# Kernel optimization log

Measured on AMD Instinct MI355X. Metric: run time of the kernel, lower is better.

## Reference

```python
import jax, jax.numpy as jnp
import numpy as np

PROJ_EPS = 1e-5   # hyperbolic_projection keeps ||x|| <= 1 - PROJ_EPS
MIN_NORM = 1e-15  # numerical floor for norms/denominators
N, D, E, L = 100000, 128, 800000, 2


def _norm(x):
    return jnp.linalg.norm(x, axis=-1, keepdims=True)


def hyperbolic_projection(x):
    n = _norm(x)
    max_n = 1.0 - PROJ_EPS
    scale = jnp.where(n > max_n, max_n / jnp.maximum(n, MIN_NORM), 1.0)
    return x * scale


def exp_map_zero(v):
    n = jnp.maximum(_norm(v), MIN_NORM)
    return jnp.tanh(n) * v / n


def log_map_zero(y):
    n = jnp.maximum(_norm(y), MIN_NORM)
    nc = jnp.clip(n, MIN_NORM, 1.0 - PROJ_EPS)
    return jnp.arctanh(nc) * y / n


def mobius_addition(u, v):
    uu = jnp.sum(u * u, -1, keepdims=True)
    vv = jnp.sum(v * v, -1, keepdims=True)
    uv = jnp.sum(u * v, -1, keepdims=True)
    num = (1.0 + 2.0 * uv + vv) * u + (1.0 - uu) * v
    den = 1.0 + 2.0 * uv + uu * vv
    return num / jnp.maximum(den, MIN_NORM)


def setup_inputs() -> dict:
    key = jax.random.key(0)
    k = jax.random.split(key, 5)
    ent = jax.random.normal(k[0], (N, D), jnp.float32) * 0.1
    W = jax.random.normal(k[1], (L, D, D), jnp.float32) * (1.0 / np.sqrt(D))
    bias = jnp.zeros((L, D), jnp.float32)
    rows = jax.random.randint(k[2], (E,), 0, N)
    cols = jax.random.randint(k[3], (E,), 0, N)
    vals = jax.random.uniform(k[4], (E,), jnp.float32) / 8.0  # ~row-normalized adj values
    return {"ent_embeddings": ent, "W": W, "bias": bias,
            "adj_rows": rows, "adj_cols": cols, "adj_vals": vals}


def _gcn_layer(x, W_l, b_l, rows, cols, vals, use_act):
    # log map to tangent at origin, linear transform
    t = log_map_zero(x)                      # [N, D]
    m = t @ W_l                              # [N, D]
    # sparse adjacency matmul: adj @ m  (COO gather-scale-scatter)
    msg = m[cols] * vals[:, None]            # [E, D]
    agg = jax.ops.segment_sum(msg, rows, num_segments=N)  # [N, D]
    h = hyperbolic_projection(exp_map_zero(agg))
    # hyperbolic bias via mobius addition
    bh = hyperbolic_projection(exp_map_zero(b_l[None, :]))  # [1, D]
    h = hyperbolic_projection(mobius_addition(h, bh))
    if use_act:
        h = hyperbolic_projection(exp_map_zero(jnp.tanh(log_map_zero(h))))
    return h


def reference(ent_embeddings, W, bias, adj_rows, adj_cols, adj_vals):
    x = hyperbolic_projection(ent_embeddings)
    for l in range(L):
        use_act = (l < L - 1)  # tanh on all but last layer
        h = _gcn_layer(x, W[l], bias[l], adj_rows, adj_cols, adj_vals, use_act)
        # mobius residual connection with previous layer output
        x = hyperbolic_projection(mobius_addition(h, x))
    return x
```

## Files before the change

kernel.cpp:

```cpp
#include <hip/hip_runtime.h>
#include <math.h>

#define D 128
#define PROJ_EPS 1e-5f
#define MAX_NN (1.0f - PROJ_EPS)
#define MIN_NORM 1e-15f
#define ROWS_PER_BLOCK 2048
#define BSHIFT 11
#define MAXB 256

struct __align__(8) Edge { int c; float v; };

typedef __attribute__((ext_vector_type(8))) short bf16x8;
typedef __attribute__((ext_vector_type(4))) float f32x4;

__device__ inline unsigned cvt_pk_bf16(float a, float b) {
    unsigned r;
    asm("v_cvt_pk_bf16_f32 %0, %1, %2" : "=v"(r) : "v"(a), "v"(b));
    return r;
}

__device__ inline float wave_sum(float v) {
#pragma unroll
    for (int off = 32; off; off >>= 1) v += __shfl_xor(v, off, 64);
    return v;
}
__device__ inline float g16sum(float v) {
#pragma unroll
    for (int off = 8; off; off >>= 1) v += __shfl_xor(v, off, 64);
    return v;
}
__device__ inline void g16sum2(float& a, float& b) {
#pragma unroll
    for (int off = 8; off; off >>= 1) {
        a += __shfl_xor(a, off, 64);
        b += __shfl_xor(b, off, 64);
    }
}
__device__ inline float frcp(float x) { return __builtin_amdgcn_rcpf(x); }
__device__ inline float fsqrt_(float x) { return __builtin_amdgcn_sqrtf(x); }
__device__ inline float tanh_pos(float x) {
    float e = __expf(-2.f * x);
    return (1.f - e) * frcp(1.f + e);
}
__device__ inline float tanh_sgn(float x) {
    float ax = fabsf(x);
    float e = __expf(-2.f * ax);
    float r = (1.f - e) * frcp(1.f + e);
    return copysignf(r, x);
}
__device__ inline float atanh_clip(float x) {
    return 0.5f * __logf((1.f + x) * frcp(1.f - x));
}

__device__ inline float2 mk2(float a, float b) { float2 r; r.x = a; r.y = b; return r; }
__device__ inline float2 bc2(float a) { return mk2(a, a); }
__device__ inline float2 pk_fma2(float2 a, float2 b, float2 c) {
    float2 d;
    asm("v_pk_fma_f32 %0, %1, %2, %3" : "=v"(d) : "v"(a), "v"(b), "v"(c));
    return d;
}
__device__ inline float2 pk_mul2(float2 a, float2 b) {
    float2 d;
    asm("v_pk_mul_f32 %0, %1, %2" : "=v"(d) : "v"(a), "v"(b));
    return d;
}
__device__ inline float2 up2(unsigned u) {
    uint2 t; t.x = u << 16; t.y = u & 0xffff0000u;
    float2 r; r.x = __uint_as_float(t.x); r.y = __uint_as_float(t.y);
    return r;
}

__global__ __launch_bounds__(256) void hist_kernel(const int* __restrict__ rows,
                                                   int* __restrict__ counts,
                                                   int* __restrict__ bucket_cnt, int e) {
    __shared__ int bhist[MAXB];
    int t = threadIdx.x;
    if (t < MAXB) bhist[t] = 0;
    __syncthreads();
    int base = blockIdx.x * 2048;
#pragma unroll
    for (int j = 0; j < 8; ++j) {
        int i = base + t * 8 + j;
        if (i < e) {
            int r = rows[i];
            atomicAdd(&counts[r], 1);
            atomicAdd(&bhist[r >> BSHIFT], 1);
        }
    }
    __syncthreads();
    if (t < MAXB && bhist[t]) atomicAdd(&bucket_cnt[t], bhist[t]);
}

__global__ __launch_bounds__(256) void partial_kernel(const int* __restrict__ counts,
                                                      int* __restrict__ partials, int n) {
    int t = threadIdx.x;
    int start = blockIdx.x * ROWS_PER_BLOCK + t * 8;
    int s = 0;
#pragma unroll
    for (int j = 0; j < 8; ++j) {
        int i = start + j;
        if (i < n) s += (counts[i] + 3) & ~3;
    }
    int lane = t & 63, wv = t >> 6;
#pragma unroll
    for (int o = 32; o; o >>= 1) s += __shfl_xor(s, o, 64);
    __shared__ int wsum[4];
    if (lane == 0) wsum[wv] = s;
    __syncthreads();
    if (t == 0) partials[blockIdx.x] = wsum[0] + wsum[1] + wsum[2] + wsum[3];
}

__global__ void scan_both(int* __restrict__ partials, int npart,
                          const int* __restrict__ bucket_cnt, int* __restrict__ bucket_cur) {
    __shared__ int buf[1024];
    int t = threadIdx.x;
    int v = (t < npart) ? partials[t] : 0;
    buf[t] = v;
    __syncthreads();
    for (int o = 1; o < 1024; o <<= 1) {
        int x = (t >= o) ? buf[t - o] : 0;
        __syncthreads();
        buf[t] += x;
        __syncthreads();
    }
    if (t < npart) partials[t] = buf[t] - v;
    __syncthreads();
    int b = (t < npart) ? bucket_cnt[t] : 0;
    buf[t] = b;
    __syncthreads();
    for (int o = 1; o < 1024; o <<= 1) {
        int x = (t >= o) ? buf[t - o] : 0;
        __syncthreads();
        buf[t] += x;
        __syncthreads();
    }
    if (t < npart) bucket_cur[t] = buf[t] - b;
}

__global__ __launch_bounds__(256) void rowptr_kernel(const int* __restrict__ counts,
                                                     const int* __restrict__ partials,
                                                     int* __restrict__ row_ptr,
                                                     int* __restrict__ cursor, int n) {
    int t = threadIdx.x;
    int start = blockIdx.x * ROWS_PER_BLOCK + t * 8;
    int c[8];
    int s = 0;
#pragma unroll
    for (int j = 0; j < 8; ++j) {
        int i = start + j;
        c[j] = (i < n) ? ((counts[i] + 3) & ~3) : 0;
        s += c[j];
    }
    int lane = t & 63, wv = t >> 6;
    int inc = s;
#pragma unroll
    for (int o = 1; o < 64; o <<= 1) {
        int tt = __shfl_up(inc, o, 64);
        if (lane >= o) inc += tt;
    }
    __shared__ int wsum[4];
    if (lane == 63) wsum[wv] = inc;
    __syncthreads();
    if (t == 0) {
        int acc = 0;
        for (int w = 0; w < 4; ++w) { int tmp = wsum[w]; wsum[w] = acc; acc += tmp; }
    }
    __syncthreads();
    int run = partials[blockIdx.x] + wsum[wv] + (inc - s);
#pragma unroll
    for (int j = 0; j < 8; ++j) {
        int i = start + j;
        if (i < n) {
            row_ptr[i] = run;
            cursor[i] = run;
            run += c[j];
            if (i == n - 1) row_ptr[n] = run;
        }
    }
}

__global__ __launch_bounds__(256) void bucket_scatter(const int* __restrict__ rows,
                                                      const int* __restrict__ cols,
                                                      const float* __restrict__ vals,
                                                      int* __restrict__ bucket_cur,
                                                      int* __restrict__ rstage,
                                                      Edge* __restrict__ estage, int e) {
    __shared__ int bhist[MAXB];
    __shared__ int bbase[MAXB];
    int t = threadIdx.x;
    if (t < MAXB) bhist[t] = 0;
    __syncthreads();
    int base = blockIdx.x * 2048;
    int b[8], lr[8];
#pragma unroll
    for (int j = 0; j < 8; ++j) {
        int i = base + t * 8 + j;
        if (i < e) {
            b[j] = rows[i] >> BSHIFT;
            lr[j] = atomicAdd(&bhist[b[j]], 1);
        } else b[j] = -1;
    }
    __syncthreads();
    if (t < MAXB) {
        int c = bhist[t];
        bbase[t] = c ? atomicAdd(&bucket_cur[t], c) : 0;
    }
    __syncthreads();
#pragma unroll
    for (int j = 0; j < 8; ++j) {
        int i = base + t * 8 + j;
        if (b[j] >= 0) {
            int pos = bbase[b[j]] + lr[j];
            rstage[pos] = rows[i];
            Edge ed; ed.c = cols[i]; ed.v = vals[i];
            estage[pos] = ed;
        }
    }
}

__global__ void scatter2(const int* __restrict__ rstage, const Edge* __restrict__ estage,
                         int* __restrict__ cursor, Edge* __restrict__ eds, int e) {
    int i = blockIdx.x * blockDim.x + threadIdx.x;
    if (i < e) {
        int r = rstage[i];
        int pos = atomicAdd(&cursor[r], 1);
        eds[pos] = estage[i];
    }
}

__global__ __launch_bounds__(256) void proj_init(const float* __restrict__ ent,
                                                 float* __restrict__ x,
                                                 float* __restrict__ logscale,
                                                 float* __restrict__ xnorm2, int n) {
    int wv = (int)((blockIdx.x * (size_t)blockDim.x + threadIdx.x) >> 6);
    int lane = threadIdx.x & 63;
    int q = lane >> 4, li = lane & 15;
    if (wv * 4 >= n) return;
    int r = wv * 4 + q;
    bool active = (r < n);
    float4 va = active ? *(const float4*)(ent + (size_t)r * D + 8 * li)
                       : make_float4(0.f, 0.f, 0.f, 0.f);
    float4 vb = active ? *(const float4*)(ent + (size_t)r * D + 8 * li + 4)
                       : make_float4(0.f, 0.f, 0.f, 0.f);
    float ss = va.x * va.x + va.y * va.y + va.z * va.z + va.w * va.w
             + vb.x * vb.x + vb.y * vb.y + vb.z * vb.z + vb.w * vb.w;
    ss = g16sum(ss);
    float nrm = fsqrt_(ss);
    float scale = (nrm > MAX_NN) ? MAX_NN * frcp(fmaxf(nrm, MIN_NORM)) : 1.0f;
    float n2 = fminf(nrm, MAX_NN);
    float nc = fminf(fmaxf(n2, MIN_NORM), MAX_NN);
    float ls = atanh_clip(nc) * frcp(fmaxf(n2, MIN_NORM));
    if (active) {
        *(float4*)(x + (size_t)r * D + 8 * li) =
            make_float4(va.x * scale, va.y * scale, va.z * scale, va.w * scale);
        *(float4*)(x + (size_t)r * D + 8 * li + 4) =
            make_float4(vb.x * scale, vb.y * scale, vb.z * scale, vb.w * scale);
        if (li == 0) { logscale[r] = ls; xnorm2[r] = n2 * n2; }
    }
}

__global__ void bias_prep(const float* __restrict__ bias, float* __restrict__ bh,
                          float* __restrict__ vvb) {
    int l = blockIdx.x;
    int lane = threadIdx.x;
    float2 b2 = *(const float2*)(bias + (size_t)l * D + 2 * lane);
    float nn = fmaxf(sqrtf(wave_sum(b2.x * b2.x + b2.y * b2.y)), MIN_NORM);
    float s = tanhf(nn) / nn;
    float bx = b2.x * s, by = b2.y * s;
    float pn = sqrtf(wave_sum(bx * bx + by * by));
    float sc = (pn > MAX_NN) ? MAX_NN / fmaxf(pn, MIN_NORM) : 1.0f;
    bx *= sc; by *= sc;
    float vv = wave_sum(bx * bx + by * by);
    *(float2*)(bh + (size_t)l * D + 2 * lane) = make_float2(bx, by);
    if (lane == 0) vvb[l] = vv;
}

__global__ __launch_bounds__(256, 3) void logmap_gemm(const float* __restrict__ x,
                                                      const float* __restrict__ logscale,
                                                      const float* __restrict__ W,
                                                      unsigned short* __restrict__ m, int n,
                                                      int ntiles) {
    __shared__ char lds[16384];
    const int t = threadIdx.x;
    const int wid = t >> 6, lane = t & 63;
    const int lcol = lane & 15, lkg = lane >> 4;
    const int colbase = wid * 32;

    bf16x8 Bh[4][2], Bl[4][2];
#pragma unroll
    for (int ki = 0; ki < 4; ++ki) {
#pragma unroll
        for (int cf = 0; cf < 2; ++cf) {
            const float* wp = W + (size_t)(ki * 32 + lkg * 8) * D + colbase + cf * 16 + lcol;
            float f[8];
#pragma unroll
            for (int e2 = 0; e2 < 8; ++e2) f[e2] = wp[(size_t)e2 * D];
            unsigned hw[4], lw[4];
#pragma unroll
            for (int p = 0; p < 4; ++p) {
                float a = f[2 * p], b = f[2 * p + 1];
                unsigned h = cvt_pk_bf16(a, b);
                float ha = __uint_as_float(h << 16);
                float hb = __uint_as_float(h & 0xffff0000u);
                hw[p] = h;
                lw[p] = cvt_pk_bf16(a - ha, b - hb);
            }
            uint4 uh = make_uint4(hw[0], hw[1], hw[2], hw[3]);
            uint4 ul = make_uint4(lw[0], lw[1], lw[2], lw[3]);
            Bh[ki][cf] = *(bf16x8*)&uh;
            Bl[ki][cf] = *(bf16x8*)&ul;
        }
    }

    for (int tile = blockIdx.x; tile < ntiles; tile += gridDim.x) {
        const int row0 = tile * 32;
        __syncthreads();
#pragma unroll
        for (int p = t; p < 512; p += 256) {
            int fi = p >> 6, ln = p & 63;
            int rf = fi >> 2, ki = fi & 3;
            int row = row0 + rf * 16 + (ln & 15);
            int k0 = ki * 32 + (ln >> 4) * 8;
            float v[8];
            if (row < n) {
                float ls = logscale[row];
                const float* xp = x + (size_t)row * D + k0;
                *(float4*)&v[0] = *(const float4*)xp;
                *(float4*)&v[4] = *(const float4*)(xp + 4);
#pragma unroll
                for (int e2 = 0; e2 < 8; ++e2) v[e2] *= ls;
            } else {
#pragma unroll
                for (int e2 = 0; e2 < 8; ++e2) v[e2] = 0.f;
            }
            unsigned hv[4], lv[4];
#pragma unroll
            for (int pp = 0; pp < 4; ++pp) {
                float a = v[2 * pp], b = v[2 * pp + 1];
                unsigned h = cvt_pk_bf16(a, b);
                float ha = __uint_as_float(h << 16);
                float hb = __uint_as_float(h & 0xffff0000u);
                hv[pp] = h;
                lv[pp] = cvt_pk_bf16(a - ha, b - hb);
            }
            *(uint4*)(lds + fi * 1024 + ln * 16) = make_uint4(hv[0], hv[1], hv[2], hv[3]);
            *(uint4*)(lds + 8192 + fi * 1024 + ln * 16) = make_uint4(lv[0], lv[1], lv[2], lv[3]);
        }
        __syncthreads();

        f32x4 acc[2][2];
#pragma unroll
        for (int cf = 0; cf < 2; ++cf)
#pragma unroll
            for (int rf = 0; rf < 2; ++rf) acc[cf][rf] = (f32x4){0.f, 0.f, 0.f, 0.f};

#pragma unroll
        for (int ki = 0; ki < 4; ++ki) {
            bf16x8 Ah[2], Al[2];
#pragma unroll
            for (int rf = 0; rf < 2; ++rf) {
                Ah[rf] = *(const bf16x8*)(lds + (rf * 4 + ki) * 1024 + lane * 16);
                Al[rf] = *(const bf16x8*)(lds + 8192 + (rf * 4 + ki) * 1024 + lane * 16);
            }
#pragma unroll
            for (int cf = 0; cf < 2; ++cf)
#pragma unroll
                for (int rf = 0; rf < 2; ++rf) {
                    acc[cf][rf] = __builtin_amdgcn_mfma_f32_16x16x32_bf16(Bh[ki][cf], Ah[rf], acc[cf][rf], 0, 0, 0);
                    acc[cf][rf] = __builtin_amdgcn_mfma_f32_16x16x32_bf16(Bl[ki][cf], Ah[rf], acc[cf][rf], 0, 0, 0);
                    acc[cf][rf] = __builtin_amdgcn_mfma_f32_16x16x32_bf16(Bh[ki][cf], Al[rf], acc[cf][rf], 0, 0, 0);
                }
        }

#pragma unroll
        for (int cf = 0; cf < 2; ++cf)
#pragma unroll
            for (int rf = 0; rf < 2; ++rf) {
                int mrow = row0 + rf * 16 + lcol;
                if (mrow < n) {
                    unsigned u0 = cvt_pk_bf16(acc[cf][rf][0], acc[cf][rf][1]);
                    unsigned u1 = cvt_pk_bf16(acc[cf][rf][2], acc[cf][rf][3]);
                    *(uint2*)(m + (size_t)mrow * D + colbase + cf * 16 + lkg * 4) =
                        make_uint2(u0, u1);
                }
            }
    }
}

__global__ __launch_bounds__(256) void aggregate(const unsigned short* __restrict__ m,
                                                 const int* __restrict__ row_ptr,
                                                 const Edge* __restrict__ eds,
                                                 const float* __restrict__ bh,
                                                 const float* __restrict__ vvb_p,
                                                 float* __restrict__ x,
                                                 float* __restrict__ logscale,
                                                 float* __restrict__ xnorm2,
                                                 int n, int use_act, int last) {
    int wv = (int)((blockIdx.x * (size_t)blockDim.x + threadIdx.x) >> 6);
    int lane = threadIdx.x & 63;
    int q = lane >> 4, li = lane & 15;
    if (wv * 4 >= n) return;
    int r = wv * 4 + q;
    bool active = (r < n);

    int beg = 0, end = 0;
    if (active) { beg = row_ptr[r]; end = row_ptr[r + 1]; }

    float vv = active ? xnorm2[r] : 0.f;
    float4 xa = active ? *(const float4*)(x + (size_t)r * D + 8 * li)
                       : make_float4(0.f, 0.f, 0.f, 0.f);
    float4 xb = active ? *(const float4*)(x + (size_t)r * D + 8 * li + 4)
                       : make_float4(0.f, 0.f, 0.f, 0.f);

    const char* mB = (const char*)m + ((size_t)li << 4);
    float2 A01 = bc2(0.f), A23 = bc2(0.f), A45 = bc2(0.f), A67 = bc2(0.f);
    int e = beg;
    for (; e + 8 <= end; e += 8) {
#pragma unroll
        for (int j = 0; j < 8; ++j) {
            Edge ee = eds[e + j];
            uint4 g = *(const uint4*)(mB + ((size_t)(unsigned)ee.c << 8));
            float2 v = bc2(ee.v);
            A01 = pk_fma2(up2(g.x), v, A01); A23 = pk_fma2(up2(g.y), v, A23);
            A45 = pk_fma2(up2(g.z), v, A45); A67 = pk_fma2(up2(g.w), v, A67);
        }
    }
    if (e < end) {
#pragma unroll
        for (int j = 0; j < 4; ++j) {
            Edge ee = eds[e + j];
            uint4 g = *(const uint4*)(mB + ((size_t)(unsigned)ee.c << 8));
            float2 v = bc2(ee.v);
            A01 = pk_fma2(up2(g.x), v, A01); A23 = pk_fma2(up2(g.y), v, A23);
            A45 = pk_fma2(up2(g.z), v, A45); A67 = pk_fma2(up2(g.w), v, A67);
        }
    }

    float4 bv0 = *(const float4*)(bh + 8 * li);
    float4 bv1 = *(const float4*)(bh + 8 * li + 4);
    float2 b01 = mk2(bv0.x, bv0.y), b23 = mk2(bv0.z, bv0.w);
    float2 b45 = mk2(bv1.x, bv1.y), b67 = mk2(bv1.z, bv1.w);
    float vvb = *vvb_p;

    float2 daa = pk_fma2(A67, A67, pk_fma2(A45, A45, pk_fma2(A23, A23, pk_mul2(A01, A01))));
    float2 dab = pk_fma2(A67, b67, pk_fma2(A45, b45, pk_fma2(A23, b23, pk_mul2(A01, b01))));
    float saa = daa.x + daa.y, sab = dab.x + dab.y;
    g16sum2(saa, sab);

    float na = fmaxf(fsqrt_(saa), MIN_NORM);
    float th = tanh_pos(na);
    float s1 = th * frcp(na);
    float nh = th;
    if (th > MAX_NN) { s1 *= MAX_NN * frcp(th); nh = MAX_NN; }
    float2 vs1 = bc2(s1);
    float2 H01 = pk_mul2(A01, vs1), H23 = pk_mul2(A23, vs1);
    float2 H45 = pk_mul2(A45, vs1), H67 = pk_mul2(A67, vs1);
    float uu = nh * nh;
    float uv = s1 * sab;

    float ca = 1.f + 2.f * uv + vvb;
    float cb = 1.f - uu;
    float den = fmaxf(1.f + 2.f * uv + uu * vvb, MIN_NORM);
    float nsq = fmaxf(ca * ca * uu + 2.f * ca * cb * uv + cb * cb * vvb, 0.f);
    float rden = frcp(den);
    float n2 = fsqrt_(nsq) * rden;
    float s2 = rden;
    if (n2 > MAX_NN) { s2 *= MAX_NN * frcp(n2); n2 = MAX_NN; }
    float2 vca = bc2(ca), vcb = bc2(cb), vs2 = bc2(s2);
    float2 P01 = pk_mul2(pk_fma2(H01, vca, pk_mul2(b01, vcb)), vs2);
    float2 P23 = pk_mul2(pk_fma2(H23, vca, pk_mul2(b23, vcb)), vs2);
    float2 P45 = pk_mul2(pk_fma2(H45, vca, pk_mul2(b45, vcb)), vs2);
    float2 P67 = pk_mul2(pk_fma2(H67, vca, pk_mul2(b67, vcb)), vs2);

    float2 xo01 = mk2(xa.x, xa.y), xo23 = mk2(xa.z, xa.w);
    float2 xo45 = mk2(xb.x, xb.y), xo67 = mk2(xb.z, xb.w);

    float2 Q01, Q23, Q45, Q67;
    float uu3, uv3;
    if (use_act) {
        float nnv = fmaxf(n2, MIN_NORM);
        float nc = fminf(fmaxf(n2, MIN_NORM), MAX_NN);
        float ls2 = atanh_clip(nc) * frcp(nnv);
        float2 vls = bc2(ls2);
        float2 Z01 = pk_mul2(P01, vls), Z23 = pk_mul2(P23, vls);
        float2 Z45 = pk_mul2(P45, vls), Z67 = pk_mul2(P67, vls);
        float2 T01 = mk2(tanh_sgn(Z01.x), tanh_sgn(Z01.y));
        float2 T23 = mk2(tanh_sgn(Z23.x), tanh_sgn(Z23.y));
        float2 T45 = mk2(tanh_sgn(Z45.x), tanh_sgn(Z45.y));
        float2 T67 = mk2(tanh_sgn(Z67.x), tanh_sgn(Z67.y));
        float2 dtt = pk_fma2(T67, T67, pk_fma2(T45, T45, pk_fma2(T23, T23, pk_mul2(T01, T01))));
        float2 dtx = pk_fma2(T67, xo67, pk_fma2(T45, xo45, pk_fma2(T23, xo23, pk_mul2(T01, xo01))));
        float stt = dtt.x + dtt.y, stx = dtx.x + dtx.y;
        g16sum2(stt, stx);
        float n3 = fmaxf(fsqrt_(stt), MIN_NORM);
        float th3 = tanh_pos(n3);
        float s3 = th3 * frcp(n3);
        float nh3 = th3;
        if (th3 > MAX_NN) { s3 *= MAX_NN * frcp(th3); nh3 = MAX_NN; }
        float2 vs3 = bc2(s3);
        Q01 = pk_mul2(T01, vs3); Q23 = pk_mul2(T23, vs3);
        Q45 = pk_mul2(T45, vs3); Q67 = pk_mul2(T67, vs3);
        uu3 = nh3 * nh3;
        uv3 = s3 * stx;
    } else {
        float2 dpx = pk_fma2(P67, xo67, pk_fma2(P45, xo45, pk_fma2(P23, xo23, pk_mul2(P01, xo01))));
        float suv = g16sum(dpx.x + dpx.y);
        Q01 = P01; Q23 = P23; Q45 = P45; Q67 = P67;
        uu3 = n2 * n2;
        uv3 = suv;
    }

    ca = 1.f + 2.f * uv3 + vv;
    cb = 1.f - uu3;
    den = fmaxf(1.f + 2.f * uv3 + uu3 * vv, MIN_NORM);
    nsq = fmaxf(ca * ca * uu3 + 2.f * ca * cb * uv3 + cb * cb * vv, 0.f);
    rden = frcp(den);
    float n4 = fsqrt_(nsq) * rden;
    float s4 = rden;
    if (n4 > MAX_NN) { s4 *= MAX_NN * frcp(n4); n4 = MAX_NN; }
    float2 vca2 = bc2(ca), vcb2 = bc2(cb), vs4 = bc2(s4);
    float2 O01 = pk_mul2(pk_fma2(Q01, vca2, pk_mul2(xo01, vcb2)), vs4);
    float2 O23 = pk_mul2(pk_fma2(Q23, vca2, pk_mul2(xo23, vcb2)), vs4);
    float2 O45 = pk_mul2(pk_fma2(Q45, vca2, pk_mul2(xo45, vcb2)), vs4);
    float2 O67 = pk_mul2(pk_fma2(Q67, vca2, pk_mul2(xo67, vcb2)), vs4);

    if (active) {
        *(float4*)(x + (size_t)r * D + 8 * li) = make_float4(O01.x, O01.y, O23.x, O23.y);
        *(float4*)(x + (size_t)r * D + 8 * li + 4) = make_float4(O45.x, O45.y, O67.x, O67.y);
        if (li == 0) {
            xnorm2[r] = n4 * n4;
            if (!last) {
                float nnv = fmaxf(n4, MIN_NORM);
                float nc = fminf(fmaxf(n4, MIN_NORM), MAX_NN);
                logscale[r] = atanh_clip(nc) * frcp(nnv);
            }
        }
    }
}

extern "C" void kernel_launch(void* const* d_in, const int* in_sizes, int n_in,
                              void* d_out, int out_size, void* d_ws, size_t ws_size,
                              hipStream_t stream) {
    const float* ent  = (const float*)d_in[0];
    const float* W    = (const float*)d_in[1];
    const float* bias = (const float*)d_in[2];
    const int* rows   = (const int*)d_in[3];
    const int* cols   = (const int*)d_in[4];
    const float* vals = (const float*)d_in[5];
    float* x = (float*)d_out;

    const int n = in_sizes[0] / D;
    const int e = in_sizes[3];
    const int nlayers = in_sizes[1] / (D * D);
    const int npart = (n + ROWS_PER_BLOCK - 1) / ROWS_PER_BLOCK;
    const int npart_e = (e + 2047) / 2048;
    const int ntiles = (n + 31) / 32;
    const size_t e_cap = (size_t)e + 3u * (size_t)n;

    char* ws = (char*)d_ws;
    size_t off = 0;
    auto alloc = [&](size_t bytes) {
        void* p = ws + off;
        off += (bytes + 255) & ~(size_t)255;
        return p;
    };
    unsigned short* m = (unsigned short*)alloc((size_t)n * D * sizeof(unsigned short));
    float* logscale = (float*)alloc((size_t)n * sizeof(float));
    float* xnorm2   = (float*)alloc((size_t)n * sizeof(float));
    int*   counts   = (int*)alloc((size_t)n * sizeof(int));
    int*   row_ptr  = (int*)alloc((size_t)(n + 1) * sizeof(int));
    int*   cursor   = (int*)alloc((size_t)n * sizeof(int));
    int*   partials = (int*)alloc((size_t)(npart > 1024 ? npart : 1024) * sizeof(int));
    int*   bucket_cnt = (int*)alloc((size_t)MAXB * sizeof(int));
    int*   bucket_cur = (int*)alloc((size_t)MAXB * sizeof(int));
    float* bhb      = (float*)alloc((size_t)nlayers * D * sizeof(float));
    float* vvb      = (float*)alloc((size_t)nlayers * sizeof(float));
    int*   rstage   = (int*)alloc((size_t)e * sizeof(int));
    Edge*  estage   = (Edge*)alloc((size_t)e * sizeof(Edge));
    Edge*  eds      = (Edge*)alloc(e_cap * sizeof(Edge));

    hipMemsetAsync(counts, 0, (size_t)n * sizeof(int), stream);
    hipMemsetAsync(bucket_cnt, 0, (size_t)MAXB * sizeof(int), stream);
    hipMemsetAsync(eds, 0, e_cap * sizeof(Edge), stream);

    hist_kernel<<<npart_e, 256, 0, stream>>>(rows, counts, bucket_cnt, e);
    partial_kernel<<<npart, 256, 0, stream>>>(counts, partials, n);
    scan_both<<<1, 1024, 0, stream>>>(partials, npart, bucket_cnt, bucket_cur);
    rowptr_kernel<<<npart, 256, 0, stream>>>(counts, partials, row_ptr, cursor, n);
    bucket_scatter<<<npart_e, 256, 0, stream>>>(rows, cols, vals, bucket_cur, rstage, estage, e);
    scatter2<<<(e + 255) / 256, 256, 0, stream>>>(rstage, estage, cursor, eds, e);

    bias_prep<<<nlayers, 64, 0, stream>>>(bias, bhb, vvb);
    proj_init<<<(n + 15) / 16, 256, 0, stream>>>(ent, x, logscale, xnorm2, n);

    for (int l = 0; l < nlayers; ++l) {
        logmap_gemm<<<782, 256, 0, stream>>>(x, logscale, W + (size_t)l * D * D, m, n, ntiles);
        int use_act = (l < nlayers - 1) ? 1 : 0;
        aggregate<<<(n + 15) / 16, 256, 0, stream>>>(m, row_ptr, eds, bhb + (size_t)l * D,
                                                     vvb + l, x, logscale, xnorm2, n,
                                                     use_act, (l == nlayers - 1) ? 1 : 0);
    }
}
```

Baseline: 275.4 us.

## Fuse GEMM into aggregation by reordering adj@(tW) to (adj@t)W

Uses associativity to aggregate the bf16 tangent vectors first and then multiply the aggregated 16-row tile by W with MFMA inside the aggregation kernel. This removes the separate logmap_gemm launch and the round trip of the m buffer. The previous layer writes the log-mapped tangent directly in bf16, double-buffered. In exchange, the per-tile GEMM adds three syncthreads per 16 rows. Inputs to the aggregation are now bf16-rounded tangents rather than bf16 GEMM outputs, which shifts where rounding error enters.

```diff
diff --git a/kernel.cpp b/kernel.cpp
--- a/kernel.cpp
+++ b/kernel.cpp
@@ -231,7 +231,7 @@
 
 __global__ __launch_bounds__(256) void proj_init(const float* __restrict__ ent,
                                                  float* __restrict__ x,
-                                                 float* __restrict__ logscale,
+                                                 unsigned short* __restrict__ t_out,
                                                  float* __restrict__ xnorm2, int n) {
     int wv = (int)((blockIdx.x * (size_t)blockDim.x + threadIdx.x) >> 6);
     int lane = threadIdx.x & 63;
@@ -252,11 +252,16 @@
     float nc = fminf(fmaxf(n2, MIN_NORM), MAX_NN);
     float ls = atanh_clip(nc) * frcp(fmaxf(n2, MIN_NORM));
     if (active) {
-        *(float4*)(x + (size_t)r * D + 8 * li) =
-            make_float4(va.x * scale, va.y * scale, va.z * scale, va.w * scale);
-        *(float4*)(x + (size_t)r * D + 8 * li + 4) =
-            make_float4(vb.x * scale, vb.y * scale, vb.z * scale, vb.w * scale);
-        if (li == 0) { logscale[r] = ls; xnorm2[r] = n2 * n2; }
+        float p0 = va.x * scale, p1 = va.y * scale, p2 = va.z * scale, p3 = va.w * scale;
+        float p4 = vb.x * scale, p5 = vb.y * scale, p6 = vb.z * scale, p7 = vb.w * scale;
+        *(float4*)(x + (size_t)r * D + 8 * li) = make_float4(p0, p1, p2, p3);
+        *(float4*)(x + (size_t)r * D + 8 * li + 4) = make_float4(p4, p5, p6, p7);
+        unsigned w0 = cvt_pk_bf16(p0 * ls, p1 * ls);
+        unsigned w1 = cvt_pk_bf16(p2 * ls, p3 * ls);
+        unsigned w2 = cvt_pk_bf16(p4 * ls, p5 * ls);
+        unsigned w3 = cvt_pk_bf16(p6 * ls, p7 * ls);
+        *(uint4*)(t_out + (size_t)r * D + 8 * li) = make_uint4(w0, w1, w2, w3);
+        if (li == 0) xnorm2[r] = n2 * n2;
     }
 }
 
@@ -276,18 +281,26 @@
     if (lane == 0) vvb[l] = vv;
 }
 
-__global__ __launch_bounds__(256, 3) void logmap_gemm(const float* __restrict__ x,
-                                                      const float* __restrict__ logscale,
-                                                      const float* __restrict__ W,
-                                                      unsigned short* __restrict__ m, int n,
-                                                      int ntiles) {
-    __shared__ char lds[16384];
+__global__ __launch_bounds__(256) void fused_layer(const unsigned short* __restrict__ t_in,
+                                                   float* __restrict__ x,
+                                                   float* __restrict__ xnorm2,
+                                                   const int* __restrict__ row_ptr,
+                                                   const Edge* __restrict__ eds,
+                                                   const float* __restrict__ bh,
+                                                   const float* __restrict__ vvb_p,
+                                                   const float* __restrict__ W,
+                                                   unsigned short* __restrict__ t_out,
+                                                   int n, int ntile, int use_act, int last) {
+    __shared__ char ufrag[8192];
+    __shared__ float gbuf[16][136];
+
     const int t = threadIdx.x;
-    const int wid = t >> 6, lane = t & 63;
+    const int w = t >> 6, lane = t & 63;
     const int lcol = lane & 15, lkg = lane >> 4;
-    const int colbase = wid * 32;
-
-    bf16x8 Bh[4][2], Bl[4][2];
+    const int q = lkg & 3, li = lcol;
+    const int colbase = w * 32;
+
+    bf16x8 Wh[4][2], Wl[4][2];
 #pragma unroll
     for (int ki = 0; ki < 4; ++ki) {
 #pragma unroll
@@ -308,132 +321,8 @@
             }
             uint4 uh = make_uint4(hw[0], hw[1], hw[2], hw[3]);
             uint4 ul = make_uint4(lw[0], lw[1], lw[2], lw[3]);
-            Bh[ki][cf] = *(bf16x8*)&uh;
-            Bl[ki][cf] = *(bf16x8*)&ul;
-        }
-    }
-
-    for (int tile = blockIdx.x; tile < ntiles; tile += gridDim.x) {
-        const int row0 = tile * 32;
-        __syncthreads();
-#pragma unroll
-        for (int p = t; p < 512; p += 256) {
-            int fi = p >> 6, ln = p & 63;
-            int rf = fi >> 2, ki = fi & 3;
-            int row = row0 + rf * 16 + (ln & 15);
-            int k0 = ki * 32 + (ln >> 4) * 8;
-            float v[8];
-            if (row < n) {
-                float ls = logscale[row];
-                const float* xp = x + (size_t)row * D + k0;
-                *(float4*)&v[0] = *(const float4*)xp;
-                *(float4*)&v[4] = *(const float4*)(xp + 4);
-#pragma unroll
-                for (int e2 = 0; e2 < 8; ++e2) v[e2] *= ls;
-            } else {
-#pragma unroll
-                for (int e2 = 0; e2 < 8; ++e2) v[e2] = 0.f;
-            }
-            unsigned hv[4], lv[4];
-#pragma unroll
-            for (int pp = 0; pp < 4; ++pp) {
-                float a = v[2 * pp], b = v[2 * pp + 1];
-                unsigned h = cvt_pk_bf16(a, b);
-                float ha = __uint_as_float(h << 16);
-                float hb = __uint_as_float(h & 0xffff0000u);
-                hv[pp] = h;
-                lv[pp] = cvt_pk_bf16(a - ha, b - hb);
-            }
-            *(uint4*)(lds + fi * 1024 + ln * 16) = make_uint4(hv[0], hv[1], hv[2], hv[3]);
-            *(uint4*)(lds + 8192 + fi * 1024 + ln * 16) = make_uint4(lv[0], lv[1], lv[2], lv[3]);
-        }
-        __syncthreads();
-
-        f32x4 acc[2][2];
-#pragma unroll
-        for (int cf = 0; cf < 2; ++cf)
-#pragma unroll
-            for (int rf = 0; rf < 2; ++rf) acc[cf][rf] = (f32x4){0.f, 0.f, 0.f, 0.f};
-
-#pragma unroll
-        for (int ki = 0; ki < 4; ++ki) {
-            bf16x8 Ah[2], Al[2];
-#pragma unroll
-            for (int rf = 0; rf < 2; ++rf) {
-                Ah[rf] = *(const bf16x8*)(lds + (rf * 4 + ki) * 1024 + lane * 16);
-                Al[rf] = *(const bf16x8*)(lds + 8192 + (rf * 4 + ki) * 1024 + lane * 16);
-            }
-#pragma unroll
-            for (int cf = 0; cf < 2; ++cf)
-#pragma unroll
-                for (int rf = 0; rf < 2; ++rf) {
-                    acc[cf][rf] = __builtin_amdgcn_mfma_f32_16x16x32_bf16(Bh[ki][cf], Ah[rf], acc[cf][rf], 0, 0, 0);
-                    acc[cf][rf] = __builtin_amdgcn_mfma_f32_16x16x32_bf16(Bl[ki][cf], Ah[rf], acc[cf][rf], 0, 0, 0);
-                    acc[cf][rf] = __builtin_amdgcn_mfma_f32_16x16x32_bf16(Bh[ki][cf], Al[rf], acc[cf][rf], 0, 0, 0);
-                }
-        }
-
-#pragma unroll
-        for (int cf = 0; cf < 2; ++cf)
-#pragma unroll
-            for (int rf = 0; rf < 2; ++rf) {
-                int mrow = row0 + rf * 16 + lcol;
-                if (mrow < n) {
-                    unsigned u0 = cvt_pk_bf16(acc[cf][rf][0], acc[cf][rf][1]);
-                    unsigned u1 = cvt_pk_bf16(acc[cf][rf][2], acc[cf][rf][3]);
-                    *(uint2*)(m + (size_t)mrow * D + colbase + cf * 16 + lkg * 4) =
-                        make_uint2(u0, u1);
-                }
-            }
-    }
-}
-
-__global__ __launch_bounds__(256) void aggregate(const unsigned short* __restrict__ m,
-                                                 const int* __restrict__ row_ptr,
-                                                 const Edge* __restrict__ eds,
-                                                 const float* __restrict__ bh,
-                                                 const float* __restrict__ vvb_p,
-                                                 float* __restrict__ x,
-                                                 float* __restrict__ logscale,
-                                                 float* __restrict__ xnorm2,
-                                                 int n, int use_act, int last) {
-    int wv = (int)((blockIdx.x * (size_t)blockDim.x + threadIdx.x) >> 6);
-    int lane = threadIdx.x & 63;
-    int q = lane >> 4, li = lane & 15;
-    if (wv * 4 >= n) return;
-    int r = wv * 4 + q;
-    bool active = (r < n);
-
-    int beg = 0, end = 0;
-    if (active) { beg = row_ptr[r]; end = row_ptr[r + 1]; }
-
-    float vv = active ? xnorm2[r] : 0.f;
-    float4 xa = active ? *(const float4*)(x + (size_t)r * D + 8 * li)
-                       : make_float4(0.f, 0.f, 0.f, 0.f);
-    float4 xb = active ? *(const float4*)(x + (size_t)r * D + 8 * li + 4)
-                       : make_float4(0.f, 0.f, 0.f, 0.f);
-
-    const char* mB = (const char*)m + ((size_t)li << 4);
-    float2 A01 = bc2(0.f), A23 = bc2(0.f), A45 = bc2(0.f), A67 = bc2(0.f);
-    int e = beg;
-    for (; e + 8 <= end; e += 8) {
-#pragma unroll
-        for (int j = 0; j < 8; ++j) {
-            Edge ee = eds[e + j];
-            uint4 g = *(const uint4*)(mB + ((size_t)(unsigned)ee.c << 8));
-            float2 v = bc2(ee.v);
-            A01 = pk_fma2(up2(g.x), v, A01); A23 = pk_fma2(up2(g.y), v, A23);
-            A45 = pk_fma2(up2(g.z), v, A45); A67 = pk_fma2(up2(g.w), v, A67);
-        }
-    }
-    if (e < end) {
-#pragma unroll
-        for (int j = 0; j < 4; ++j) {
-            Edge ee = eds[e + j];
-            uint4 g = *(const uint4*)(mB + ((size_t)(unsigned)ee.c << 8));
-            float2 v = bc2(ee.v);
-            A01 = pk_fma2(up2(g.x), v, A01); A23 = pk_fma2(up2(g.y), v, A23);
-            A45 = pk_fma2(up2(g.z), v, A45); A67 = pk_fma2(up2(g.w), v, A67);
+            Wh[ki][cf] = *(bf16x8*)&uh;
+            Wl[ki][cf] = *(bf16x8*)&ul;
         }
     }
 
@@ -443,99 +332,184 @@
     float2 b45 = mk2(bv1.x, bv1.y), b67 = mk2(bv1.z, bv1.w);
     float vvb = *vvb_p;
 
-    float2 daa = pk_fma2(A67, A67, pk_fma2(A45, A45, pk_fma2(A23, A23, pk_mul2(A01, A01))));
-    float2 dab = pk_fma2(A67, b67, pk_fma2(A45, b45, pk_fma2(A23, b23, pk_mul2(A01, b01))));
-    float saa = daa.x + daa.y, sab = dab.x + dab.y;
-    g16sum2(saa, sab);
-
-    float na = fmaxf(fsqrt_(saa), MIN_NORM);
-    float th = tanh_pos(na);
-    float s1 = th * frcp(na);
-    float nh = th;
-    if (th > MAX_NN) { s1 *= MAX_NN * frcp(th); nh = MAX_NN; }
-    float2 vs1 = bc2(s1);
-    float2 H01 = pk_mul2(A01, vs1), H23 = pk_mul2(A23, vs1);
-    float2 H45 = pk_mul2(A45, vs1), H67 = pk_mul2(A67, vs1);
-    float uu = nh * nh;
-    float uv = s1 * sab;
-
-    float ca = 1.f + 2.f * uv + vvb;
-    float cb = 1.f - uu;
-    float den = fmaxf(1.f + 2.f * uv + uu * vvb, MIN_NORM);
-    float nsq = fmaxf(ca * ca * uu + 2.f * ca * cb * uv + cb * cb * vvb, 0.f);
-    float rden = frcp(den);
-    float n2 = fsqrt_(nsq) * rden;
-    float s2 = rden;
-    if (n2 > MAX_NN) { s2 *= MAX_NN * frcp(n2); n2 = MAX_NN; }
-    float2 vca = bc2(ca), vcb = bc2(cb), vs2 = bc2(s2);
-    float2 P01 = pk_mul2(pk_fma2(H01, vca, pk_mul2(b01, vcb)), vs2);
-    float2 P23 = pk_mul2(pk_fma2(H23, vca, pk_mul2(b23, vcb)), vs2);
-    float2 P45 = pk_mul2(pk_fma2(H45, vca, pk_mul2(b45, vcb)), vs2);
-    float2 P67 = pk_mul2(pk_fma2(H67, vca, pk_mul2(b67, vcb)), vs2);
-
-    float2 xo01 = mk2(xa.x, xa.y), xo23 = mk2(xa.z, xa.w);
-    float2 xo45 = mk2(xb.x, xb.y), xo67 = mk2(xb.z, xb.w);
-
-    float2 Q01, Q23, Q45, Q67;
-    float uu3, uv3;
-    if (use_act) {
-        float nnv = fmaxf(n2, MIN_NORM);
-        float nc = fminf(fmaxf(n2, MIN_NORM), MAX_NN);
-        float ls2 = atanh_clip(nc) * frcp(nnv);
-        float2 vls = bc2(ls2);
-        float2 Z01 = pk_mul2(P01, vls), Z23 = pk_mul2(P23, vls);
-        float2 Z45 = pk_mul2(P45, vls), Z67 = pk_mul2(P67, vls);
-        float2 T01 = mk2(tanh_sgn(Z01.x), tanh_sgn(Z01.y));
-        float2 T23 = mk2(tanh_sgn(Z23.x), tanh_sgn(Z23.y));
-        float2 T45 = mk2(tanh_sgn(Z45.x), tanh_sgn(Z45.y));
-        float2 T67 = mk2(tanh_sgn(Z67.x), tanh_sgn(Z67.y));
-        float2 dtt = pk_fma2(T67, T67, pk_fma2(T45, T45, pk_fma2(T23, T23, pk_mul2(T01, T01))));
-        float2 dtx = pk_fma2(T67, xo67, pk_fma2(T45, xo45, pk_fma2(T23, xo23, pk_mul2(T01, xo01))));
-        float stt = dtt.x + dtt.y, stx = dtx.x + dtx.y;
-        g16sum2(stt, stx);
-        float n3 = fmaxf(fsqrt_(stt), MIN_NORM);
-        float th3 = tanh_pos(n3);
-        float s3 = th3 * frcp(n3);
-        float nh3 = th3;
-        if (th3 > MAX_NN) { s3 *= MAX_NN * frcp(th3); nh3 = MAX_NN; }
-        float2 vs3 = bc2(s3);
-        Q01 = pk_mul2(T01, vs3); Q23 = pk_mul2(T23, vs3);
-        Q45 = pk_mul2(T45, vs3); Q67 = pk_mul2(T67, vs3);
-        uu3 = nh3 * nh3;
-        uv3 = s3 * stx;
-    } else {
-        float2 dpx = pk_fma2(P67, xo67, pk_fma2(P45, xo45, pk_fma2(P23, xo23, pk_mul2(P01, xo01))));
-        float suv = g16sum(dpx.x + dpx.y);
-        Q01 = P01; Q23 = P23; Q45 = P45; Q67 = P67;
-        uu3 = n2 * n2;
-        uv3 = suv;
-    }
-
-    ca = 1.f + 2.f * uv3 + vv;
-    cb = 1.f - uu3;
-    den = fmaxf(1.f + 2.f * uv3 + uu3 * vv, MIN_NORM);
-    nsq = fmaxf(ca * ca * uu3 + 2.f * ca * cb * uv3 + cb * cb * vv, 0.f);
-    rden = frcp(den);
-    float n4 = fsqrt_(nsq) * rden;
-    float s4 = rden;
-    if (n4 > MAX_NN) { s4 *= MAX_NN * frcp(n4); n4 = MAX_NN; }
-    float2 vca2 = bc2(ca), vcb2 = bc2(cb), vs4 = bc2(s4);
-    float2 O01 = pk_mul2(pk_fma2(Q01, vca2, pk_mul2(xo01, vcb2)), vs4);
-    float2 O23 = pk_mul2(pk_fma2(Q23, vca2, pk_mul2(xo23, vcb2)), vs4);
-    float2 O45 = pk_mul2(pk_fma2(Q45, vca2, pk_mul2(xo45, vcb2)), vs4);
-    float2 O67 = pk_mul2(pk_fma2(Q67, vca2, pk_mul2(xo67, vcb2)), vs4);
-
-    if (active) {
-        *(float4*)(x + (size_t)r * D + 8 * li) = make_float4(O01.x, O01.y, O23.x, O23.y);
-        *(float4*)(x + (size_t)r * D + 8 * li + 4) = make_float4(O45.x, O45.y, O67.x, O67.y);
-        if (li == 0) {
-            xnorm2[r] = n4 * n4;
+    const char* tB = (const char*)t_in + ((size_t)li << 4);
+
+    for (int tile = blockIdx.x; tile < ntile; tile += gridDim.x) {
+        int r = tile * 16 + w * 4 + q;
+        bool active = (r < n);
+        int beg = 0, end = 0;
+        if (active) { beg = row_ptr[r]; end = row_ptr[r + 1]; }
+
+        float vv = active ? xnorm2[r] : 0.f;
+        float4 xa = active ? *(const float4*)(x + (size_t)r * D + 8 * li)
+                           : make_float4(0.f, 0.f, 0.f, 0.f);
+        float4 xb = active ? *(const float4*)(x + (size_t)r * D + 8 * li + 4)
+                           : make_float4(0.f, 0.f, 0.f, 0.f);
+
+        float2 A01 = bc2(0.f), A23 = bc2(0.f), A45 = bc2(0.f), A67 = bc2(0.f);
+        int e = beg;
+        for (; e + 8 <= end; e += 8) {
+#pragma unroll
+            for (int j = 0; j < 8; ++j) {
+                Edge ee = eds[e + j];
+                uint4 g = *(const uint4*)(tB + ((size_t)(unsigned)ee.c << 8));
+                float2 v = bc2(ee.v);
+                A01 = pk_fma2(up2(g.x), v, A01); A23 = pk_fma2(up2(g.y), v, A23);
+                A45 = pk_fma2(up2(g.z), v, A45); A67 = pk_fma2(up2(g.w), v, A67);
+            }
+        }
+        if (e < end) {
+#pragma unroll
+            for (int j = 0; j < 4; ++j) {
+                Edge ee = eds[e + j];
+                uint4 g = *(const uint4*)(tB + ((size_t)(unsigned)ee.c << 8));
+                float2 v = bc2(ee.v);
+                A01 = pk_fma2(up2(g.x), v, A01); A23 = pk_fma2(up2(g.y), v, A23);
+                A45 = pk_fma2(up2(g.z), v, A45); A67 = pk_fma2(up2(g.w), v, A67);
+            }
+        }
+
+        {
+            unsigned h0 = cvt_pk_bf16(A01.x, A01.y);
+            unsigned h1 = cvt_pk_bf16(A23.x, A23.y);
+            unsigned h2 = cvt_pk_bf16(A45.x, A45.y);
+            unsigned h3 = cvt_pk_bf16(A67.x, A67.y);
+            unsigned l0 = cvt_pk_bf16(A01.x - __uint_as_float(h0 << 16),
+                                      A01.y - __uint_as_float(h0 & 0xffff0000u));
+            unsigned l1 = cvt_pk_bf16(A23.x - __uint_as_float(h1 << 16),
+                                      A23.y - __uint_as_float(h1 & 0xffff0000u));
+            unsigned l2 = cvt_pk_bf16(A45.x - __uint_as_float(h2 << 16),
+                                      A45.y - __uint_as_float(h2 & 0xffff0000u));
+            unsigned l3 = cvt_pk_bf16(A67.x - __uint_as_float(h3 << 16),
+                                      A67.y - __uint_as_float(h3 & 0xffff0000u));
+            int fi = li >> 2;
+            int Lf = (w * 4 + q) + 16 * (li & 3);
+            *(uint4*)(ufrag + fi * 1024 + Lf * 16) = make_uint4(h0, h1, h2, h3);
+            *(uint4*)(ufrag + 4096 + fi * 1024 + Lf * 16) = make_uint4(l0, l1, l2, l3);
+        }
+        __syncthreads();
+
+        f32x4 acc0 = (f32x4){0.f, 0.f, 0.f, 0.f};
+        f32x4 acc1 = (f32x4){0.f, 0.f, 0.f, 0.f};
+#pragma unroll
+        for (int ki = 0; ki < 4; ++ki) {
+            bf16x8 Uh = *(const bf16x8*)(ufrag + ki * 1024 + lane * 16);
+            bf16x8 Ul = *(const bf16x8*)(ufrag + 4096 + ki * 1024 + lane * 16);
+            acc0 = __builtin_amdgcn_mfma_f32_16x16x32_bf16(Wh[ki][0], Uh, acc0, 0, 0, 0);
+            acc0 = __builtin_amdgcn_mfma_f32_16x16x32_bf16(Wl[ki][0], Uh, acc0, 0, 0, 0);
+            acc0 = __builtin_amdgcn_mfma_f32_16x16x32_bf16(Wh[ki][0], Ul, acc0, 0, 0, 0);
+            acc1 = __builtin_amdgcn_mfma_f32_16x16x32_bf16(Wh[ki][1], Uh, acc1, 0, 0, 0);
+            acc1 = __builtin_amdgcn_mfma_f32_16x16x32_bf16(Wl[ki][1], Uh, acc1, 0, 0, 0);
+            acc1 = __builtin_amdgcn_mfma_f32_16x16x32_bf16(Wh[ki][1], Ul, acc1, 0, 0, 0);
+        }
+        *(float4*)&gbuf[lcol][colbase + lkg * 4] = *(float4*)&acc0;
+        *(float4*)&gbuf[lcol][colbase + 16 + lkg * 4] = *(float4*)&acc1;
+        __syncthreads();
+
+        int rr = w * 4 + q;
+        float4 ga = *(const float4*)&gbuf[rr][8 * li];
+        float4 gb = *(const float4*)&gbuf[rr][8 * li + 4];
+        float2 G01 = mk2(ga.x, ga.y), G23 = mk2(ga.z, ga.w);
+        float2 G45 = mk2(gb.x, gb.y), G67 = mk2(gb.z, gb.w);
+
+        float2 daa = pk_fma2(G67, G67, pk_fma2(G45, G45, pk_fma2(G23, G23, pk_mul2(G01, G01))));
+        float2 dab = pk_fma2(G67, b67, pk_fma2(G45, b45, pk_fma2(G23, b23, pk_mul2(G01, b01))));
+        float saa = daa.x + daa.y, sab = dab.x + dab.y;
+        g16sum2(saa, sab);
+
+        float na = fmaxf(fsqrt_(saa), MIN_NORM);
+        float th = tanh_pos(na);
+        float s1 = th * frcp(na);
+        float nh = th;
+        if (th > MAX_NN) { s1 *= MAX_NN * frcp(th); nh = MAX_NN; }
+        float2 vs1 = bc2(s1);
+        float2 H01 = pk_mul2(G01, vs1), H23 = pk_mul2(G23, vs1);
+        float2 H45 = pk_mul2(G45, vs1), H67 = pk_mul2(G67, vs1);
+        float uu = nh * nh;
+        float uv = s1 * sab;
+
+        float ca = 1.f + 2.f * uv + vvb;
+        float cb = 1.f - uu;
+        float den = fmaxf(1.f + 2.f * uv + uu * vvb, MIN_NORM);
+        float nsq = fmaxf(ca * ca * uu + 2.f * ca * cb * uv + cb * cb * vvb, 0.f);
+        float rden = frcp(den);
+        float n2 = fsqrt_(nsq) * rden;
+        float s2 = rden;
+        if (n2 > MAX_NN) { s2 *= MAX_NN * frcp(n2); n2 = MAX_NN; }
+        float2 vca = bc2(ca), vcb = bc2(cb), vs2 = bc2(s2);
+        float2 P01 = pk_mul2(pk_fma2(H01, vca, pk_mul2(b01, vcb)), vs2);
+        float2 P23 = pk_mul2(pk_fma2(H23, vca, pk_mul2(b23, vcb)), vs2);
+        float2 P45 = pk_mul2(pk_fma2(H45, vca, pk_mul2(b45, vcb)), vs2);
+        float2 P67 = pk_mul2(pk_fma2(H67, vca, pk_mul2(b67, vcb)), vs2);
+
+        float2 xo01 = mk2(xa.x, xa.y), xo23 = mk2(xa.z, xa.w);
+        float2 xo45 = mk2(xb.x, xb.y), xo67 = mk2(xb.z, xb.w);
+
+        float2 Q01, Q23, Q45, Q67;
+        float uu3, uv3;
+        if (use_act) {
+            float nnv = fmaxf(n2, MIN_NORM);
+            float nc = fminf(fmaxf(n2, MIN_NORM), MAX_NN);
+            float ls2 = atanh_clip(nc) * frcp(nnv);
+            float2 vls = bc2(ls2);
+            float2 Z01 = pk_mul2(P01, vls), Z23 = pk_mul2(P23, vls);
+            float2 Z45 = pk_mul2(P45, vls), Z67 = pk_mul2(P67, vls);
+            float2 T01 = mk2(tanh_sgn(Z01.x), tanh_sgn(Z01.y));
+            float2 T23 = mk2(tanh_sgn(Z23.x), tanh_sgn(Z23.y));
+            float2 T45 = mk2(tanh_sgn(Z45.x), tanh_sgn(Z45.y));
+            float2 T67 = mk2(tanh_sgn(Z67.x), tanh_sgn(Z67.y));
+            float2 dtt = pk_fma2(T67, T67, pk_fma2(T45, T45, pk_fma2(T23, T23, pk_mul2(T01, T01))));
+            float2 dtx = pk_fma2(T67, xo67, pk_fma2(T45, xo45, pk_fma2(T23, xo23, pk_mul2(T01, xo01))));
+            float stt = dtt.x + dtt.y, stx = dtx.x + dtx.y;
+            g16sum2(stt, stx);
+            float n3 = fmaxf(fsqrt_(stt), MIN_NORM);
+            float th3 = tanh_pos(n3);
+            float s3 = th3 * frcp(n3);
+            float nh3 = th3;
+            if (th3 > MAX_NN) { s3 *= MAX_NN * frcp(th3); nh3 = MAX_NN; }
+            float2 vs3 = bc2(s3);
+            Q01 = pk_mul2(T01, vs3); Q23 = pk_mul2(T23, vs3);
+            Q45 = pk_mul2(T45, vs3); Q67 = pk_mul2(T67, vs3);
+            uu3 = nh3 * nh3;
+            uv3 = s3 * stx;
+        } else {
+            float2 dpx = pk_fma2(P67, xo67, pk_fma2(P45, xo45, pk_fma2(P23, xo23, pk_mul2(P01, xo01))));
+            float suv = g16sum(dpx.x + dpx.y);
+            Q01 = P01; Q23 = P23; Q45 = P45; Q67 = P67;
+            uu3 = n2 * n2;
+            uv3 = suv;
+        }
+
+        ca = 1.f + 2.f * uv3 + vv;
+        cb = 1.f - uu3;
+        den = fmaxf(1.f + 2.f * uv3 + uu3 * vv, MIN_NORM);
+        nsq = fmaxf(ca * ca * uu3 + 2.f * ca * cb * uv3 + cb * cb * vv, 0.f);
+        rden = frcp(den);
+        float n4 = fsqrt_(nsq) * rden;
+        float s4 = rden;
+        if (n4 > MAX_NN) { s4 *= MAX_NN * frcp(n4); n4 = MAX_NN; }
+        float2 vca2 = bc2(ca), vcb2 = bc2(cb), vs4 = bc2(s4);
+        float2 O01 = pk_mul2(pk_fma2(Q01, vca2, pk_mul2(xo01, vcb2)), vs4);
+        float2 O23 = pk_mul2(pk_fma2(Q23, vca2, pk_mul2(xo23, vcb2)), vs4);
+        float2 O45 = pk_mul2(pk_fma2(Q45, vca2, pk_mul2(xo45, vcb2)), vs4);
+        float2 O67 = pk_mul2(pk_fma2(Q67, vca2, pk_mul2(xo67, vcb2)), vs4);
+
+        if (active) {
+            *(float4*)(x + (size_t)r * D + 8 * li) = make_float4(O01.x, O01.y, O23.x, O23.y);
+            *(float4*)(x + (size_t)r * D + 8 * li + 4) = make_float4(O45.x, O45.y, O67.x, O67.y);
+            if (li == 0) xnorm2[r] = n4 * n4;
             if (!last) {
                 float nnv = fmaxf(n4, MIN_NORM);
-                float nc = fminf(fmaxf(n4, MIN_NORM), MAX_NN);
-                logscale[r] = atanh_clip(nc) * frcp(nnv);
+                float nc = fminf(nnv, MAX_NN);
+                float ls = atanh_clip(nc) * frcp(nnv);
+                unsigned w0 = cvt_pk_bf16(O01.x * ls, O01.y * ls);
+                unsigned w1 = cvt_pk_bf16(O23.x * ls, O23.y * ls);
+                unsigned w2 = cvt_pk_bf16(O45.x * ls, O45.y * ls);
+                unsigned w3 = cvt_pk_bf16(O67.x * ls, O67.y * ls);
+                *(uint4*)(t_out + (size_t)r * D + 8 * li) = make_uint4(w0, w1, w2, w3);
             }
         }
+        __syncthreads();
     }
 }
 
@@ -555,7 +529,7 @@
     const int nlayers = in_sizes[1] / (D * D);
     const int npart = (n + ROWS_PER_BLOCK - 1) / ROWS_PER_BLOCK;
     const int npart_e = (e + 2047) / 2048;
-    const int ntiles = (n + 31) / 32;
+    const int ntile = (n + 15) / 16;
     const size_t e_cap = (size_t)e + 3u * (size_t)n;
 
     char* ws = (char*)d_ws;
@@ -565,8 +539,8 @@
         off += (bytes + 255) & ~(size_t)255;
         return p;
     };
-    unsigned short* m = (unsigned short*)alloc((size_t)n * D * sizeof(unsigned short));
-    float* logscale = (float*)alloc((size_t)n * sizeof(float));
+    unsigned short* t0 = (unsigned short*)alloc((size_t)n * D * sizeof(unsigned short));
+    unsigned short* t1 = (unsigned short*)alloc((size_t)n * D * sizeof(unsigned short));
     float* xnorm2   = (float*)alloc((size_t)n * sizeof(float));
     int*   counts   = (int*)alloc((size_t)n * sizeof(int));
     int*   row_ptr  = (int*)alloc((size_t)(n + 1) * sizeof(int));
@@ -592,13 +566,17 @@
     scatter2<<<(e + 255) / 256, 256, 0, stream>>>(rstage, estage, cursor, eds, e);
 
     bias_prep<<<nlayers, 64, 0, stream>>>(bias, bhb, vvb);
-    proj_init<<<(n + 15) / 16, 256, 0, stream>>>(ent, x, logscale, xnorm2, n);
-
+    proj_init<<<(n + 15) / 16, 256, 0, stream>>>(ent, x, t0, xnorm2, n);
+
+    int grid = ntile < 2048 ? ntile : 2048;
     for (int l = 0; l < nlayers; ++l) {
-        logmap_gemm<<<782, 256, 0, stream>>>(x, logscale, W + (size_t)l * D * D, m, n, ntiles);
+        const unsigned short* tin = (l & 1) ? t1 : t0;
+        unsigned short* tout = (l & 1) ? t0 : t1;
         int use_act = (l < nlayers - 1) ? 1 : 0;
-        aggregate<<<(n + 15) / 16, 256, 0, stream>>>(m, row_ptr, eds, bhb + (size_t)l * D,
-                                                     vvb + l, x, logscale, xnorm2, n,
-                                                     use_act, (l == nlayers - 1) ? 1 : 0);
-    }
-}
+        int last = (l == nlayers - 1) ? 1 : 0;
+        fused_layer<<<grid, 256, 0, stream>>>(tin, x, xnorm2, row_ptr, eds,
+                                              bhb + (size_t)l * D, vvb + l,
+                                              W + (size_t)l * D * D, tout,
+                                              n, ntile, use_act, last);
+    }
+}
```

Result: slower. 337.8 us (+22.7%).
